# Kernel optimization log

Hardware: AMD Instinct MI355X
Metric: run time of the kernel (lower is better)

Reference implementation:

```python
import jax, jax.numpy as jnp
import numpy as np

NH = 8          # num_heads
EMB = 256       # embed_dim
HD = EMB // NH  # head_dim
NV = 6          # num_views
NL = 4          # num_fmap_levels
NP = 4          # num_ref_points
NZ = 4          # num_z_ref_points
OFFSET_SCALE = 1.0
SHAPES = [(64, 64), (32, 32), (16, 16), (8, 8)]
SLEN = sum(h * w for h, w in SHAPES)  # 5440


def setup_inputs() -> dict:
    key = jax.random.key(0)
    ks = jax.random.split(key, 9)
    N, Q = 1, 1600
    A = NH * NV * NL * NP * NZ  # total sampling slots per query
    s = 0.02
    return {
        "queries": jax.random.normal(ks[0], (N, Q, EMB), jnp.float32),
        # pre-normalized reference points in [-1, 1] (normalize_ref_points=False path)
        "ref_points": jax.random.uniform(ks[1], (N, Q, NV, NL, NZ, 2), jnp.float32, -1.0, 1.0),
        "value": jax.random.normal(ks[2], (N, NV, SLEN, EMB), jnp.float32),
        "value_spatial_shapes": jnp.asarray(SHAPES, jnp.int32),
        "Wv": jax.random.normal(ks[3], (EMB, EMB), jnp.float32) * s,
        "Woff": jax.random.normal(ks[4], (A * 2, EMB), jnp.float32) * s,
        "boff": jnp.zeros((A * 2,), jnp.float32),
        "Wattn": jax.random.normal(ks[5], (A, EMB), jnp.float32) * s,
        "battn": jnp.zeros((A,), jnp.float32),
        "Wout": jax.random.normal(ks[6], (EMB, EMB), jnp.float32) * s,
    }


def _forward(queries, ref_points, value, shapes_np, Wv, Woff, boff, Wattn, battn, Wout):
    N, Q, C = queries.shape
    # sampling offsets: tanh-bounded, scaled
    offs = jnp.tanh(queries @ Woff.T + boff) * OFFSET_SCALE
    offs = offs.reshape(N, Q, NH, NV, NL, NP, NZ, 2)
    # attention weights: softmax over all (view, level, point, z) slots per head
    attn = (queries @ Wattn.T + battn).reshape(N, Q, NH, NV * NL * NP * NZ)
    attn = jax.nn.softmax(attn, axis=-1).reshape(N, Q, NH, NV, NL, NP, NZ)
    # value projection, split heads: (N, V, H, S, hd)
    val = (value @ Wv.T).reshape(N, NV, -1, NH, HD)
    val = jnp.transpose(val, (0, 1, 3, 2, 4))
    # sampling locations, clamped to [-1, 1] (grid_sample normalized coords)
    locs = jnp.clip(ref_points[:, :, None, :, :, None, :, :] + offs, -1.0, 1.0)  # (N,Q,H,V,L,P,Z,2)
    locs = jnp.transpose(locs, (0, 3, 2, 4, 1, 5, 6, 7))   # (N,V,H,L,Q,P,Z,2)
    attn_t = jnp.transpose(attn, (0, 3, 2, 4, 1, 5, 6))     # (N,V,H,L,Q,P,Z)

    out = jnp.zeros((N, Q, NH, HD), queries.dtype)
    start = 0
    for l in range(NL):
        Hl, Wl = int(shapes_np[l, 0]), int(shapes_np[l, 1])
        S = Hl * Wl
        fmap = val[:, :, :, start:start + S, :]  # (N,V,H,S,hd)
        g = locs[:, :, :, l].reshape(N, NV, NH, Q * NP * NZ, 2)
        # align_corners=True mapping; coords are clamped so zero-padding never triggers
        x = (g[..., 0] + 1.0) * 0.5 * (Wl - 1)
        y = (g[..., 1] + 1.0) * 0.5 * (Hl - 1)
        x0 = jnp.floor(x); y0 = jnp.floor(y)
        wx = x - x0; wy = y - y0
        x0i = jnp.clip(x0.astype(jnp.int32), 0, Wl - 1)
        y0i = jnp.clip(y0.astype(jnp.int32), 0, Hl - 1)
        x1i = jnp.clip(x0i + 1, 0, Wl - 1)
        y1i = jnp.clip(y0i + 1, 0, Hl - 1)

        def gat(yi, xi):
            return jnp.take_along_axis(fmap, (yi * Wl + xi)[..., None], axis=3)

        samp = (((1 - wy) * (1 - wx))[..., None] * gat(y0i, x0i)
                + ((1 - wy) * wx)[..., None] * gat(y0i, x1i)
                + (wy * (1 - wx))[..., None] * gat(y1i, x0i)
                + (wy * wx)[..., None] * gat(y1i, x1i))  # (N,V,H,QPZ,hd)
        samp = samp.reshape(N, NV, NH, Q, NP, NZ, HD)
        out = out + jnp.einsum('nvhqpzd,nvhqpz->nqhd', samp, attn_t[:, :, :, l])
        start += S

    out = out.reshape(N, Q, C)
    return out @ Wout.T  # out_fc (dropout is identity at inference)


def reference(queries, ref_points, value, value_spatial_shapes, Wv, Woff, boff, Wattn, battn, Wout):
    shapes_np = np.asarray(value_spatial_shapes)
    return _forward(queries, ref_points, value, shapes_np, Wv, Woff, boff, Wattn, battn, Wout)
```

## Files before the change

kernel.cpp:

```cpp
#include <hip/hip_runtime.h>
#include <hip/hip_bf16.h>
#include <math.h>

#define NHh   8
#define EMB   256
#define HDd   32
#define NVv   6
#define SLENs 5440
#define QQ    1600
#define A_ATTN 3072
#define A_OFF  6144

typedef _Float16 half8 __attribute__((ext_vector_type(8)));
typedef __attribute__((ext_vector_type(4))) float f32x4;

__device__ __forceinline__ unsigned short f2bf(float f) {
  __hip_bfloat16 h = __float2bfloat16(f);
  return *(unsigned short*)&h;
}
__device__ __forceinline__ unsigned short f2h(float f) {
  _Float16 h = (_Float16)f;
  return __builtin_bit_cast(unsigned short, h);
}
__device__ __forceinline__ float h2f(unsigned short u) {
  return (float)__builtin_bit_cast(_Float16, u);
}

__device__ __forceinline__ void dma16(const unsigned short* g, unsigned short* l) {
  __builtin_amdgcn_global_load_lds(
      (const __attribute__((address_space(1))) unsigned int*)g,
      (__attribute__((address_space(3))) unsigned int*)l, 16, 0, 0);
}

#define FMAMIX_LO(accv, dat, uw)                                              \
  asm("v_fma_mix_f32 %0, %1, %2, %0 op_sel:[0,1,0] op_sel_hi:[1,1,0]"         \
      : "+v"(accv) : "v"(dat), "v"(uw))
#define FMAMIX_HI(accv, dat, uw)                                              \
  asm("v_fma_mix_f32 %0, %1, %2, %0 op_sel:[1,1,0] op_sel_hi:[1,1,0]"         \
      : "+v"(accv) : "v"(dat), "v"(uw))

#define GEMM_COMPUTE2(LAx, LBx)                                               \
  {                                                                           \
    half8 fa[2], fb[2];                                                       \
    _Pragma("unroll") for (int i = 0; i < 2; ++i) {                           \
      int ar = (wm + i * 16 + l16) * 32 + quad * 8;                           \
      int br = (wn + i * 16 + l16) * 32 + quad * 8;                           \
      fa[i] = *(const half8*)&LAx[ar];                                        \
      fb[i] = *(const half8*)&LBx[br];                                        \
    }                                                                         \
    _Pragma("unroll") for (int i = 0; i < 2; ++i)                             \
      _Pragma("unroll") for (int j = 0; j < 2; ++j)                           \
        acc[i][j] = __builtin_amdgcn_mfma_f32_16x16x32_f16(                   \
            fa[i], fb[j], acc[i][j], 0, 0, 0);                                \
  }

__global__ __launch_bounds__(256) void split_h_kernel(
    const float* __restrict__ q, const float* __restrict__ value,
    const float* __restrict__ Woff, const float* __restrict__ Wattn,
    const float* __restrict__ Wv, const float* __restrict__ Wout,
    unsigned short* __restrict__ q16, unsigned short* __restrict__ v16,
    unsigned short* __restrict__ Wq16, unsigned short* __restrict__ Wv16,
    unsigned short* __restrict__ Wout16) {
  int i4 = blockIdx.x * 256 + threadIdx.x;
  const float* src; unsigned short* dst; int sloc; int dloc;
  if      (i4 < 102400)  { src = q;     dst = q16;    sloc = i4;           dloc = sloc; }
  else if (i4 < 2191360) { src = value; dst = v16;    sloc = i4 - 102400;  dloc = sloc; }
  else if (i4 < 2584576) { src = Woff;  dst = Wq16;   sloc = i4 - 2191360; dloc = sloc; }
  else if (i4 < 2781184) { src = Wattn; dst = Wq16;   sloc = i4 - 2584576; dloc = sloc + 393216; }
  else if (i4 < 2797568) { src = Wv;    dst = Wv16;   sloc = i4 - 2781184; dloc = sloc; }
  else                   { src = Wout;  dst = Wout16; sloc = i4 - 2797568; dloc = sloc; }
  float4 x = ((const float4*)src)[sloc];
  ushort4 hh;
  hh.x = f2h(x.x); hh.y = f2h(x.y); hh.z = f2h(x.z); hh.w = f2h(x.w);
  ((ushort4*)dst)[dloc] = hh;
}

__global__ __launch_bounds__(256) void gemm23_kernel(
    const unsigned short* __restrict__ q16, const unsigned short* __restrict__ Wq16,
    const unsigned short* __restrict__ v16, const unsigned short* __restrict__ Wv16,
    const float* __restrict__ boff, const float* __restrict__ battn,
    unsigned short* __restrict__ offs16, unsigned short* __restrict__ attn16,
    unsigned short* __restrict__ val_t) {
  const int bid = blockIdx.x;
  const unsigned short *A, *B;
  int M, bm, bn;
  bool isVal;
  if (bid < 936) {
    int x = bid & 7, i = bid >> 3;
    int nt = x * 9 + (i % 9), mt = i / 9;
    A = q16;  B = Wq16;  M = QQ;
    bn = nt * 128;  bm = mt * 128;  isVal = false;
  } else {
    int b2 = bid - 936;
    A = v16;  B = Wv16;  M = NVv * SLENs;
    bn = (b2 & 1) * 128;  bm = (b2 >> 1) * 128;  isVal = true;
  }
  const int K = EMB;

  const int tid = threadIdx.x;
  const int lane = tid & 63, w = tid >> 6;
  const int wm = (w & 1) * 64, wn = (w >> 1) * 64;
  const int l16 = lane & 15, quad = lane >> 4;

  const unsigned short* Arow[4];
  const unsigned short* Brow[4];
#pragma unroll
  for (int i = 0; i < 4; ++i)
    Arow[i] = A + (size_t)min(bm + wm + i * 16 + l16, M - 1) * K + quad * 8;
#pragma unroll
  for (int j = 0; j < 4; ++j)
    Brow[j] = B + (size_t)(bn + wn + j * 16 + l16) * K + quad * 8;

  f32x4 acc[4][4] = {};

#pragma unroll
  for (int k0 = 0; k0 < 256; k0 += 32) {
    half8 fa[4], fb[4];
#pragma unroll
    for (int i = 0; i < 4; ++i) fa[i] = *(const half8*)(Arow[i] + k0);
#pragma unroll
    for (int j = 0; j < 4; ++j) fb[j] = *(const half8*)(Brow[j] + k0);
#pragma unroll
    for (int i = 0; i < 4; ++i)
#pragma unroll
      for (int j = 0; j < 4; ++j)
        acc[i][j] = __builtin_amdgcn_mfma_f32_16x16x32_f16(fa[i], fb[j], acc[i][j], 0, 0, 0);
  }

#pragma unroll
  for (int j = 0; j < 4; ++j) {
    int n = bn + wn + j * 16 + l16;
    float bv = 0.f;
    bool dotanh = false;
    if (!isVal) {
      if (n < A_OFF) { bv = boff[n]; dotanh = true; }
      else bv = battn[n - A_OFF];
    }
#pragma unroll
    for (int i = 0; i < 4; ++i) {
      int mbase = bm + wm + i * 16 + quad * 4;
#pragma unroll
      for (int reg = 0; reg < 4; ++reg) {
        int m = mbase + reg;
        if (m >= M) continue;
        float c = acc[i][j][reg] + bv;
        if (isVal) {
          int vv = m / SLENs;
          int s = m - vv * SLENs;
          int hh2 = n >> 5, dd = n & 31;
          val_t[((size_t)(vv * 8 + hh2) * SLENs + s) * 32 + dd] = f2h(c);
        } else if (dotanh) {
          float t = __expf(2.f * c);
          c = 1.f - 2.f / (t + 1.f);
          offs16[(size_t)m * A_OFF + n] = f2h(c);
        } else {
          attn16[(size_t)m * A_ATTN + (n - A_OFF)] = f2h(c);
        }
      }
    }
  }
}

__global__ __launch_bounds__(256) void gemmh0_kernel(
    const unsigned short* __restrict__ A, const unsigned short* __restrict__ B,
    float* __restrict__ C, int M, int N, int K) {
  __shared__ unsigned short LA0[64 * 32], LA1[64 * 32], LA2[64 * 32], LA3[64 * 32];
  __shared__ unsigned short LB0[64 * 32], LB1[64 * 32], LB2[64 * 32], LB3[64 * 32];

  const int tid = threadIdx.x;
  const int bm = blockIdx.y * 64, bn = blockIdx.x * 64;
  const int lane = tid & 63, w = tid >> 6;
  const int wm = (w & 1) * 32, wn = (w >> 1) * 32;
  const int l16 = lane & 15, quad = lane >> 4;

  const int r0 = tid >> 2, s0 = (tid & 3) * 8;
  const size_t a0 = (size_t)min(bm + r0, M - 1) * K + s0;
  const size_t b0o = (size_t)(bn + r0) * K + s0;
  const int l0 = tid * 8;

  f32x4 acc[2][2] = {};

#pragma unroll
  for (int k0 = 0; k0 < K; k0 += 128) {
    dma16(&A[a0 + k0],       &LA0[l0]);
    dma16(&A[a0 + k0 + 32],  &LA1[l0]);
    dma16(&A[a0 + k0 + 64],  &LA2[l0]);
    dma16(&A[a0 + k0 + 96],  &LA3[l0]);
    dma16(&B[b0o + k0],      &LB0[l0]);
    dma16(&B[b0o + k0 + 32], &LB1[l0]);
    dma16(&B[b0o + k0 + 64], &LB2[l0]);
    dma16(&B[b0o + k0 + 96], &LB3[l0]);
    __syncthreads();
    GEMM_COMPUTE2(LA0, LB0);
    GEMM_COMPUTE2(LA1, LB1);
    GEMM_COMPUTE2(LA2, LB2);
    GEMM_COMPUTE2(LA3, LB3);
    __syncthreads();
  }

#pragma unroll
  for (int j = 0; j < 2; ++j) {
    int n = bn + wn + j * 16 + l16;
#pragma unroll
    for (int i = 0; i < 2; ++i) {
      int mbase = bm + wm + i * 16 + quad * 4;
#pragma unroll
      for (int reg = 0; reg < 4; ++reg) {
        int m = mbase + reg;
        if (m >= M) continue;
        C[(size_t)m * N + n] = acc[i][j][reg];
      }
    }
  }
}

__global__ __launch_bounds__(256) void sample_kernel(
    const float* __restrict__ ref, const unsigned short* __restrict__ offs16,
    const unsigned short* __restrict__ attn16,
    const unsigned short* __restrict__ val_t,
    unsigned short* __restrict__ op16) {
  __shared__ int4 Lrec[4][384];

  const int h   = blockIdx.x & 7;
  const int qt  = blockIdx.x >> 3;
  const int wid = threadIdx.x >> 6;
  const int lane = threadIdx.x & 63;
  const int q   = qt * 4 + wid;
  const int row = q * 8 + h;

  {
    const unsigned short* ap = attn16 + (size_t)row * 384;
    float vals[6];
    float mx = -1e30f;
#pragma unroll
    for (int i = 0; i < 6; ++i) { vals[i] = h2f(ap[lane + i * 64]); mx = fmaxf(mx, vals[i]); }
#pragma unroll
    for (int o = 32; o > 0; o >>= 1) mx = fmaxf(mx, __shfl_xor(mx, o, 64));
    float s = 0.f;
#pragma unroll
    for (int i = 0; i < 6; ++i) { vals[i] = __expf(vals[i] - mx); s += vals[i]; }
#pragma unroll
    for (int o = 32; o > 0; o >>= 1) s += __shfl_xor(s, o, 64);
    const float inv = 1.0f / s;

    const int l = (lane >> 4) & 3;
    const int z = lane & 3;
    const int Wl = 64 >> l;
    const int start = (l == 0) ? 0 : (l == 1 ? 4096 : (l == 2 ? 5120 : 5376));
    const float sc = 0.5f * (float)(Wl - 1);
    const unsigned int* op = (const unsigned int*)offs16 + (size_t)row * 384;
    const float* rq = ref + (size_t)q * (NVv * 4 * 4 * 2);

#pragma unroll 1
    for (int v = 0; v < 6; ++v) {
      int j = v * 64 + lane;
      float w = vals[v] * inv;
      unsigned int oxy = op[j];
      float ox = h2f((unsigned short)(oxy & 0xFFFF));
      float oy = h2f((unsigned short)(oxy >> 16));
      const float* rp = rq + ((v * 4 + l) * 4 + z) * 2;
      float rx = rp[0], ry = rp[1];
      float x = fminf(1.f, fmaxf(-1.f, rx + ox));
      float y = fminf(1.f, fmaxf(-1.f, ry + oy));
      float xp = (x + 1.f) * sc, yp = (y + 1.f) * sc;
      float x0f = floorf(xp), y0f = floorf(yp);
      int x0 = (int)x0f, y0 = (int)y0f;
      float wx = xp - x0f, wy = yp - y0f;
      unsigned i00 = (unsigned)(start + y0 * Wl + x0);
      unsigned dxe = (x0 + 1 < Wl) ? 1u : 0u;
      unsigned dye = (y0 + 1 < Wl) ? (unsigned)Wl : 0u;
      unsigned i10 = i00 + dye;
      float wxw = wx * w, wmx = w - wxw;
      float w01 = wxw * (1.f - wy), w11 = wxw * wy;
      float w00 = wmx * (1.f - wy), w10 = wmx * wy;
      Lrec[wid][j] = make_int4(
          (int)(i00         | ((unsigned)f2h(w00) << 16)),
          (int)((i00 + dxe) | ((unsigned)f2h(w01) << 16)),
          (int)(i10         | ((unsigned)f2h(w10) << 16)),
          (int)((i10 + dxe) | ((unsigned)f2h(w11) << 16)));
    }
  }

  const int cb  = (lane >> 2) & 3;
  const int e16 = (lane & 3) << 4;
  const int r   = lane >> 4;

  const unsigned* Lw = (const unsigned*)&Lrec[wid][0];

  float acc[8] = {};

#pragma unroll 1
  for (int v = 0; v < 6; ++v) {
    const char* sb = (const char*)val_t + (size_t)(v * 8 + h) * (SLENs * 64);
    const int rbase = v * 64 + r;
#pragma unroll 8
    for (int t = 0; t < 16; ++t) {
      int ri = rbase + t * 4;
      unsigned u = Lw[ri * 4 + cb];
      int voff = ((int)(u & 0xFFFFu) << 6) + e16;
      uint4 d = *(const uint4*)(sb + voff);
      FMAMIX_LO(acc[0], d.x, u);  FMAMIX_HI(acc[1], d.x, u);
      FMAMIX_LO(acc[2], d.y, u);  FMAMIX_HI(acc[3], d.y, u);
      FMAMIX_LO(acc[4], d.z, u);  FMAMIX_HI(acc[5], d.z, u);
      FMAMIX_LO(acc[6], d.w, u);  FMAMIX_HI(acc[7], d.w, u);
    }
  }

#pragma unroll
  for (int m = 4; m <= 32; m <<= 1)
#pragma unroll
    for (int j = 0; j < 8; ++j) acc[j] += __shfl_xor(acc[j], m, 64);

  if (lane < 4) {
    int off = q * EMB + h * 32 + lane * 8;
    ushort4 h0, h1;
    h0.x = f2h(acc[0]); h0.y = f2h(acc[1]); h0.z = f2h(acc[2]); h0.w = f2h(acc[3]);
    h1.x = f2h(acc[4]); h1.y = f2h(acc[5]); h1.z = f2h(acc[6]); h1.w = f2h(acc[7]);
    *(ushort4*)&op16[off] = h0;  *(ushort4*)&op16[off + 4] = h1;
  }
}

extern "C" void kernel_launch(void* const* d_in, const int* in_sizes, int n_in,
                              void* d_out, int out_size, void* d_ws, size_t ws_size,
                              hipStream_t stream) {
  const float* queries    = (const float*)d_in[0];
  const float* ref_points = (const float*)d_in[1];
  const float* value      = (const float*)d_in[2];
  const float* Wv    = (const float*)d_in[4];
  const float* Woff  = (const float*)d_in[5];
  const float* boff  = (const float*)d_in[6];
  const float* Wattn = (const float*)d_in[7];
  const float* battn = (const float*)d_in[8];
  const float* Wout  = (const float*)d_in[9];
  float* out = (float*)d_out;

  char* W = (char*)d_ws;
  unsigned short* offs16 = (unsigned short*)(W + 0);
  unsigned short* attn16 = (unsigned short*)(W + 19660800);
  unsigned short* val_t  = (unsigned short*)(W + 29491200);
  unsigned short* q16    = (unsigned short*)(W + 46202880);
  unsigned short* v16    = (unsigned short*)(W + 47022080);
  unsigned short* Wq16   = (unsigned short*)(W + 63733760);
  unsigned short* Wv16   = (unsigned short*)(W + 68452352);
  unsigned short* Wout16 = (unsigned short*)(W + 68583424);
  unsigned short* op16   = (unsigned short*)(W + 68714496);

  dim3 blk(256);

  split_h_kernel<<<10992, blk, 0, stream>>>(
      queries, value, Woff, Wattn, Wv, Wout, q16, v16, Wq16, Wv16, Wout16);
  gemm23_kernel<<<1446, blk, 0, stream>>>(
      q16, Wq16, v16, Wv16, boff, battn, offs16, attn16, val_t);
  sample_kernel<<<QQ * NHh / 4, blk, 0, stream>>>(
      ref_points, offs16, attn16, val_t, op16);
  gemmh0_kernel<<<dim3(EMB / 64, QQ / 64), blk, 0, stream>>>(
      op16, Wout16, out, QQ, EMB, EMB);
}
```

Before: 223.2 us.

## Stage GEMM tiles through LDS with direct loads and shrink tiles to 64x64

The fused offset/attention/value-projection GEMM now loads A and B tiles into shared memory with direct global-to-LDS copies (dma16) and computes from LDS. Previously each wave read its fragments straight from global memory. Block tiles drop from 128x128 to 64x64, so the launch grows from 1446 to 5640 blocks. The intent is better load coalescing and more parallelism, at the cost of lower per-block arithmetic intensity and extra barriers.

```diff
diff --git a/kernel.cpp b/kernel.cpp
--- a/kernel.cpp
+++ b/kernel.cpp
@@ -81,54 +81,57 @@
     const float* __restrict__ boff, const float* __restrict__ battn,
     unsigned short* __restrict__ offs16, unsigned short* __restrict__ attn16,
     unsigned short* __restrict__ val_t) {
+  __shared__ unsigned short LA0[64 * 32], LA1[64 * 32], LA2[64 * 32], LA3[64 * 32];
+  __shared__ unsigned short LB0[64 * 32], LB1[64 * 32], LB2[64 * 32], LB3[64 * 32];
+
   const int bid = blockIdx.x;
   const unsigned short *A, *B;
   int M, bm, bn;
   bool isVal;
-  if (bid < 936) {
+  if (bid < 3600) {
     int x = bid & 7, i = bid >> 3;
-    int nt = x * 9 + (i % 9), mt = i / 9;
+    int nt = x * 18 + (i % 18), mt = i / 18;
     A = q16;  B = Wq16;  M = QQ;
-    bn = nt * 128;  bm = mt * 128;  isVal = false;
+    bn = nt * 64;  bm = mt * 64;  isVal = false;
   } else {
-    int b2 = bid - 936;
+    int b2 = bid - 3600;
     A = v16;  B = Wv16;  M = NVv * SLENs;
-    bn = (b2 & 1) * 128;  bm = (b2 >> 1) * 128;  isVal = true;
+    bn = (b2 & 3) * 64;  bm = (b2 >> 2) * 64;  isVal = true;
   }
   const int K = EMB;
 
   const int tid = threadIdx.x;
   const int lane = tid & 63, w = tid >> 6;
-  const int wm = (w & 1) * 64, wn = (w >> 1) * 64;
+  const int wm = (w & 1) * 32, wn = (w >> 1) * 32;
   const int l16 = lane & 15, quad = lane >> 4;
 
-  const unsigned short* Arow[4];
-  const unsigned short* Brow[4];
-#pragma unroll
-  for (int i = 0; i < 4; ++i)
-    Arow[i] = A + (size_t)min(bm + wm + i * 16 + l16, M - 1) * K + quad * 8;
-#pragma unroll
-  for (int j = 0; j < 4; ++j)
-    Brow[j] = B + (size_t)(bn + wn + j * 16 + l16) * K + quad * 8;
-
-  f32x4 acc[4][4] = {};
-
-#pragma unroll
-  for (int k0 = 0; k0 < 256; k0 += 32) {
-    half8 fa[4], fb[4];
-#pragma unroll
-    for (int i = 0; i < 4; ++i) fa[i] = *(const half8*)(Arow[i] + k0);
-#pragma unroll
-    for (int j = 0; j < 4; ++j) fb[j] = *(const half8*)(Brow[j] + k0);
-#pragma unroll
-    for (int i = 0; i < 4; ++i)
-#pragma unroll
-      for (int j = 0; j < 4; ++j)
-        acc[i][j] = __builtin_amdgcn_mfma_f32_16x16x32_f16(fa[i], fb[j], acc[i][j], 0, 0, 0);
-  }
-
-#pragma unroll
-  for (int j = 0; j < 4; ++j) {
+  const int r0 = tid >> 2, s0 = (tid & 3) * 8;
+  const size_t a0 = (size_t)min(bm + r0, M - 1) * K + s0;
+  const size_t b0o = (size_t)(bn + r0) * K + s0;
+  const int l0 = tid * 8;
+
+  f32x4 acc[2][2] = {};
+
+#pragma unroll
+  for (int k0 = 0; k0 < K; k0 += 128) {
+    dma16(&A[a0 + k0],       &LA0[l0]);
+    dma16(&A[a0 + k0 + 32],  &LA1[l0]);
+    dma16(&A[a0 + k0 + 64],  &LA2[l0]);
+    dma16(&A[a0 + k0 + 96],  &LA3[l0]);
+    dma16(&B[b0o + k0],      &LB0[l0]);
+    dma16(&B[b0o + k0 + 32], &LB1[l0]);
+    dma16(&B[b0o + k0 + 64], &LB2[l0]);
+    dma16(&B[b0o + k0 + 96], &LB3[l0]);
+    __syncthreads();
+    GEMM_COMPUTE2(LA0, LB0);
+    GEMM_COMPUTE2(LA1, LB1);
+    GEMM_COMPUTE2(LA2, LB2);
+    GEMM_COMPUTE2(LA3, LB3);
+    __syncthreads();
+  }
+
+#pragma unroll
+  for (int j = 0; j < 2; ++j) {
     int n = bn + wn + j * 16 + l16;
     float bv = 0.f;
     bool dotanh = false;
@@ -137,7 +140,7 @@
       else bv = battn[n - A_OFF];
     }
 #pragma unroll
-    for (int i = 0; i < 4; ++i) {
+    for (int i = 0; i < 2; ++i) {
       int mbase = bm + wm + i * 16 + quad * 4;
 #pragma unroll
       for (int reg = 0; reg < 4; ++reg) {
@@ -349,7 +352,7 @@
 
   split_h_kernel<<<10992, blk, 0, stream>>>(
       queries, value, Woff, Wattn, Wv, Wout, q16, v16, Wq16, Wv16, Wout16);
-  gemm23_kernel<<<1446, blk, 0, stream>>>(
+  gemm23_kernel<<<5640, blk, 0, stream>>>(
       q16, Wq16, v16, Wv16, boff, battn, offs16, attn16, val_t);
   sample_kernel<<<QQ * NHh / 4, blk, 0, stream>>>(
       ref_points, offs16, attn16, val_t, op16);
```

New measurement: 197.4 us, median of 2. 1.13x faster.
